# Optimization experiments

Measured on AMD Instinct MI355X. Metric: run time of the kernel, lower is better.

Reference implementation:

```python
import jax, jax.numpy as jnp
import numpy as np

NUM_EXPERTS = 8
RANK = 16
TOP_K = 2
SCALING = 32.0 / RANK  # alpha / rank = 2.0
IN_F = 2048
OUT_F = 2048


def setup_inputs() -> dict:
    key = jax.random.key(0)
    k1, k2, k3, k4, k5 = jax.random.split(key, 5)
    B, T = 4, 2048
    x = jax.random.normal(k1, (B, T, IN_F), dtype=jnp.float32)
    # kaiming-uniform-ish scales
    bound_w = 1.0 / np.sqrt(IN_F)
    weight = jax.random.uniform(k2, (OUT_F, IN_F), jnp.float32, -bound_w, bound_w)
    lora_A = jax.random.uniform(k3, (NUM_EXPERTS, RANK, IN_F), jnp.float32, -bound_w, bound_w)
    # lora_B is zero-initialized in the module; use small random values so the
    # expert path is numerically non-trivial for kernel correctness testing.
    lora_B = 0.02 * jax.random.normal(k4, (NUM_EXPERTS, OUT_F, RANK), dtype=jnp.float32)
    router_w = jax.random.uniform(k5, (NUM_EXPERTS, IN_F), jnp.float32, -bound_w, bound_w)
    return {"x": x, "weight": weight, "lora_A": lora_A, "lora_B": lora_B, "router_w": router_w}


def reference(x, weight, lora_A, lora_B, router_w):
    B, T, D = x.shape
    N = B * T
    # base dense projection: [B,T,O]
    base = jnp.einsum('btd,od->bto', x, weight)
    # routing
    logits = jnp.einsum('btd,ed->bte', x, router_w)
    probs = jax.nn.softmax(logits, axis=-1)
    topk_vals, topk_idx = jax.lax.top_k(probs, TOP_K)          # [B,T,K]
    topk_vals = topk_vals / topk_vals.sum(axis=-1, keepdims=True)
    # dense per-token expert weights: zero for non-selected experts -> same math
    # as the per-k gather loop (top_k indices are distinct).
    w_dense = jnp.zeros((N, NUM_EXPERTS), dtype=x.dtype).at[
        jnp.arange(N)[:, None], topk_idx.reshape(N, TOP_K)
    ].set(topk_vals.reshape(N, TOP_K))                          # [N,E]
    x_flat = x.reshape(N, D)
    # low-rank expert path: Ax [N,E,r] is tiny (E*r=128), then weighted combine
    Ax = jnp.einsum('nd,erd->ner', x_flat, lora_A)
    expert_out = jnp.einsum('ner,ne,eor->no', Ax, w_dense, lora_B) * SCALING
    return base + expert_out.reshape(B, T, OUT_F)
```

## Files before the change

### kernel.cpp

```cpp
#include <hip/hip_runtime.h>
#include <hip/hip_bf16.h>
#include <stdint.h>

#define IN_F   2048
#define OUT_F  2048
#define NTOK   8192
#define KAUG   2176
#define RANKE  128
#define SCALING 2.0f
#define NT64   34
#define NITER  17

typedef float  f32x4 __attribute__((ext_vector_type(4)));
typedef __bf16 bf16x8 __attribute__((ext_vector_type(8)));

#define GLOAD(g, l) __builtin_amdgcn_global_load_lds(                                   \
    (const __attribute__((address_space(1))) unsigned int*)(g),                          \
    (__attribute__((address_space(3))) unsigned int*)(l), 16, 0, 0)
#define PIN()    asm volatile("" ::: "memory")
#define BAR()    __builtin_amdgcn_s_barrier()
#define WAITL()  asm volatile("s_waitcnt lgkmcnt(0)" ::: "memory")
#define WAITV0() asm volatile("s_waitcnt vmcnt(0)" ::: "memory")
#define WAITV4() asm volatile("s_waitcnt vmcnt(4)" ::: "memory")
#define WAITV5() asm volatile("s_waitcnt vmcnt(5)" ::: "memory")
#define SB0()    __builtin_amdgcn_sched_barrier(0)

__device__ __forceinline__ unsigned short f2b(float f) {
  union { float f; unsigned u; } v; v.f = f;
  return (unsigned short)((v.u + 0x7FFFu + ((v.u >> 16) & 1u)) >> 16);
}

__device__ __forceinline__ uint4 pack8(float4 a, float4 b) {
  uint4 p;
  p.x = f2b(a.x) | ((unsigned)f2b(a.y) << 16);
  p.y = f2b(a.z) | ((unsigned)f2b(a.w) << 16);
  p.z = f2b(b.x) | ((unsigned)f2b(b.y) << 16);
  p.w = f2b(b.z) | ((unsigned)f2b(b.w) << 16);
  return p;
}

__device__ __forceinline__ uint2 pack4(float4 a) {
  uint2 p;
  p.x = f2b(a.x) | ((unsigned)f2b(a.y) << 16);
  p.y = f2b(a.z) | ((unsigned)f2b(a.w) << 16);
  return p;
}

__global__ __launch_bounds__(256)
void k_pre(const float* __restrict__ x, const float* __restrict__ rw,
           const float* __restrict__ wt, const float* __restrict__ lb,
           const float* __restrict__ la,
           unsigned short* __restrict__ Ap, float* __restrict__ wsc,
           unsigned short* __restrict__ Bp, unsigned short* __restrict__ Ac) {
  const int bid = blockIdx.x;
  const int t = threadIdx.x;

  if (bid >= 3072) {
    const int r0 = (bid - 3072) * 16;
    #pragma unroll
    for (int j = 0; j < 16; ++j) {
      int ch = j * 256 + t;
      int row = r0 + (ch >> 8), col8 = ch & 255;
      const float4* src = (const float4*)(la + (size_t)row * IN_F + col8 * 8);
      *(uint4*)(Ac + (size_t)row * IN_F + col8 * 8) = pack8(src[0], src[1]);
    }
    return;
  }
  if (bid >= 1024) {
    const int o = bid - 1024;
    const int c = t * 8;
    const float4* src = (const float4*)(wt + (size_t)o * IN_F + c);
    *(uint4*)(Bp + (size_t)o * KAUG + c) = pack8(src[0], src[1]);
    if (t < RANKE) {
      float v = lb[((size_t)(t >> 4) * OUT_F + o) * 16 + (t & 15)];
      Bp[(size_t)o * KAUG + IN_F + t] = f2b(v);
    }
    return;
  }

  const int w = t >> 6, l = t & 63;
  const int n0 = bid * 8 + w * 2;

  float4 xr[2][8];
  #pragma unroll
  for (int ti = 0; ti < 2; ++ti) {
    const float4* xp = (const float4*)(x + (size_t)(n0 + ti) * IN_F);
    uint2* dst = (uint2*)(Ap + (size_t)(n0 + ti) * KAUG);
    #pragma unroll
    for (int j = 0; j < 8; ++j) {
      float4 a = xp[j * 64 + l];
      xr[ti][j] = a;
      dst[j * 64 + l] = pack4(a);
    }
  }
  float acc[2][8];
  #pragma unroll
  for (int ti = 0; ti < 2; ++ti)
    #pragma unroll
    for (int e = 0; e < 8; ++e) acc[ti][e] = 0.f;
  #pragma unroll
  for (int e = 0; e < 8; ++e) {
    const float4* wp = (const float4*)(rw + (size_t)e * IN_F);
    #pragma unroll
    for (int j = 0; j < 8; ++j) {
      float4 b = wp[j * 64 + l];
      #pragma unroll
      for (int ti = 0; ti < 2; ++ti)
        acc[ti][e] += xr[ti][j].x * b.x + xr[ti][j].y * b.y +
                      xr[ti][j].z * b.z + xr[ti][j].w * b.w;
    }
  }
  #pragma unroll
  for (int ti = 0; ti < 2; ++ti)
    #pragma unroll
    for (int e = 0; e < 8; ++e) {
      #pragma unroll
      for (int msk = 1; msk <= 32; msk <<= 1) acc[ti][e] += __shfl_xor(acc[ti][e], msk);
    }
  #pragma unroll
  for (int ti = 0; ti < 2; ++ti) {
    float m = acc[ti][0];
    #pragma unroll
    for (int e = 1; e < 8; ++e) m = fmaxf(m, acc[ti][e]);
    float ex[8], dn = 0.f;
    #pragma unroll
    for (int e = 0; e < 8; ++e) { ex[e] = expf(acc[ti][e] - m); dn += ex[e]; }
    float inv = 1.f / dn;
    float v1 = -1.f; int i1 = 0;
    #pragma unroll
    for (int e = 0; e < 8; ++e) {
      float p = ex[e] * inv;
      if (p > v1) { v1 = p; i1 = e; }
    }
    float v2 = -1.f; int i2 = 0;
    #pragma unroll
    for (int e = 0; e < 8; ++e) {
      float p = ex[e] * inv;
      if (e != i1 && p > v2) { v2 = p; i2 = e; }
    }
    if ((l >> 3) == ti) {
      int e = l & 7;
      float wsum = v1 + v2;
      float wv = (e == i1) ? (v1 / wsum) : ((e == i2) ? (v2 / wsum) : 0.f);
      wsc[(size_t)(n0 + ti) * 8 + e] = wv * SCALING;
    }
  }
}

__global__ __launch_bounds__(256)
void k_lora(const unsigned short* __restrict__ Ap, const unsigned short* __restrict__ Ac,
            const float* __restrict__ wsc, unsigned short* __restrict__ Vout) {
  __shared__ alignas(16) unsigned short LA[3 * 2048];
  __shared__ alignas(16) unsigned short LB[3 * 8192];
  const int t = threadIdx.x, bm = blockIdx.x;
  const int w = t >> 6, l = t & 63;
  const int lr = l & 15, lq = l >> 4, lx = l & 7;
  const unsigned short* Ablk = Ap + (size_t)bm * 32 * KAUG;
  const int rr = t >> 3, cs = t & 7;
  const int sc = cs ^ (rr & 7);

  f32x4 acc[2][2];
  #pragma unroll
  for (int i = 0; i < 2; ++i)
    #pragma unroll
    for (int j = 0; j < 2; ++j) acc[i][j] = f32x4{0.f, 0.f, 0.f, 0.f};

  auto stg = [&](int buf, int kt) {
    GLOAD(Ablk + (size_t)rr * KAUG + kt * 64 + sc * 8, LA + buf * 2048 + w * 512);
    #pragma unroll
    for (int r = 0; r < 4; ++r)
      GLOAD(Ac + (size_t)(r * 32 + rr) * IN_F + kt * 64 + sc * 8,
            LB + buf * 8192 + r * 2048 + w * 512);
  };

  const int as0 = (lq ^ lx) * 8, as1 = ((4 + lq) ^ lx) * 8;

  stg(0, 0); stg(1, 1);
  for (int kt = 0; kt < 32; ++kt) {
    if (kt == 31) { WAITV0(); } else { WAITV5(); }
    PIN(); BAR();
    if (kt + 2 < 32) stg((kt + 2) % 3, kt + 2);
    const int buf = kt % 3;
    bf16x8 aF[2][2], bF[2][2];
    #pragma unroll
    for (int mi = 0; mi < 2; ++mi) {
      aF[mi][0] = *(const bf16x8*)(LA + buf * 2048 + lr * 64 + mi * 1024 + as0);
      aF[mi][1] = *(const bf16x8*)(LA + buf * 2048 + lr * 64 + mi * 1024 + as1);
    }
    #pragma unroll
    for (int ni = 0; ni < 2; ++ni) {
      bF[ni][0] = *(const bf16x8*)(LB + buf * 8192 + w * 2048 + lr * 64 + ni * 1024 + as0);
      bF[ni][1] = *(const bf16x8*)(LB + buf * 8192 + w * 2048 + lr * 64 + ni * 1024 + as1);
    }
    #pragma unroll
    for (int mi = 0; mi < 2; ++mi)
      #pragma unroll
      for (int ni = 0; ni < 2; ++ni)
        #pragma unroll
        for (int ks = 0; ks < 2; ++ks)
          acc[mi][ni] = __builtin_amdgcn_mfma_f32_16x16x32_bf16(aF[mi][ks], bF[ni][ks], acc[mi][ni], 0, 0, 0);
  }

  #pragma unroll
  for (int mi = 0; mi < 2; ++mi)
    #pragma unroll
    for (int ni = 0; ni < 2; ++ni)
      #pragma unroll
      for (int j = 0; j < 4; ++j) {
        int row = bm * 32 + mi * 16 + lq * 4 + j;
        int col = w * 32 + ni * 16 + lr;
        float sg = wsc[row * 8 + (col >> 4)];
        Vout[(size_t)row * KAUG + col] = f2b(acc[mi][ni][j] * sg);
      }
}

__global__ __launch_bounds__(512, 2)
void k_main(const unsigned short* __restrict__ A, const unsigned short* __restrict__ B,
            float* __restrict__ out) {
  __shared__ alignas(16) unsigned short LDS[65536];

  const int tid = threadIdx.x;
  const int id = blockIdx.x;
  const int wg = (id & 7) * 32 + (id >> 3);
  const int bn = wg >> 5, bm = wg & 31;
  const int w = tid >> 6, l = tid & 63;
  const int wr = w >> 2, wc = w & 3;
  const int lr = l & 15, lq = l >> 4, lx = l & 7;

  const unsigned short* Ablk = A + (size_t)bm * 256 * KAUG;
  const unsigned short* Bblk = B + (size_t)bn * 256 * KAUG;

  const size_t gofs0 = (size_t)(tid >> 3) * KAUG + (size_t)(((tid & 7) ^ ((tid >> 3) & 7)) * 8);
  const size_t gofs1 = (size_t)((tid + 512) >> 3) * KAUG +
                       (size_t)((((tid + 512) & 7) ^ (((tid + 512) >> 3) & 7)) * 8);
  unsigned short* const ldsW = LDS + w * 512;

  const int arow = wr * 128 + lr, brow = wc * 64 + lr;
  const int sl0 = (lq ^ lx) * 8, sl1 = ((4 + lq) ^ lx) * 8;

  f32x4 acc[8][4];
  #pragma unroll
  for (int i = 0; i < 8; ++i)
    #pragma unroll
    for (int j = 0; j < 4; ++j) acc[i][j] = f32x4{0.f, 0.f, 0.f, 0.f};
  bf16x8 aF[4][2], bF[4][2];

  auto stage = [&](int isB, int half, int kt) {
    if (kt >= NT64) return;
    const unsigned short* g = (isB ? Bblk : Ablk) + (size_t)(half * 128) * KAUG + (size_t)kt * 64;
    unsigned short* ld = ldsW + isB * 32768 + (kt & 1) * 16384 + half * 8192;
    GLOAD(g + gofs0, ld);
    GLOAD(g + gofs1, ld + 4096);
  };

#define QUAD(MQ, NQ)                                                                     \
  do {                                                                                   \
    _Pragma("unroll") for (int mi_ = 0; mi_ < 4; ++mi_)                                  \
    _Pragma("unroll") for (int ni_ = 0; ni_ < 2; ++ni_)                                  \
    _Pragma("unroll") for (int ks_ = 0; ks_ < 2; ++ks_)                                  \
      acc[(MQ)*4 + mi_][(NQ)*2 + ni_] = __builtin_amdgcn_mfma_f32_16x16x32_bf16(         \
          aF[mi_][ks_], bF[(NQ)*2 + ni_][ks_], acc[(MQ)*4 + mi_][(NQ)*2 + ni_],          \
          0, 0, 0);                                                                      \
  } while (0)

  stage(1, 0, 0); stage(1, 1, 0); stage(0, 0, 0); stage(0, 1, 0);
  stage(1, 0, 1); stage(1, 1, 1);
  WAITV4(); PIN(); BAR();

  for (int i = 0; i < NITER; ++i) {
    const int k1 = 2 * i + 1;
    const int a0 = arow * 64,   b0 = 32768 + brow * 64;
    const int a1 = a0 + 16384,  b1 = b0 + 16384;

    #pragma unroll
    for (int mi = 0; mi < 4; ++mi) {
      aF[mi][0] = *(const bf16x8*)(LDS + a0 + mi * 1024 + sl0);
      aF[mi][1] = *(const bf16x8*)(LDS + a0 + mi * 1024 + sl1);
    }
    #pragma unroll
    for (int ni = 0; ni < 2; ++ni) {
      bF[ni][0] = *(const bf16x8*)(LDS + b0 + ni * 1024 + sl0);
      bF[ni][1] = *(const bf16x8*)(LDS + b0 + ni * 1024 + sl1);
    }
    stage(0, 0, k1);
    PIN(); WAITL(); SB0();
    __builtin_amdgcn_s_setprio(1); QUAD(0, 0); __builtin_amdgcn_s_setprio(0);
    PIN(); BAR();
    #pragma unroll
    for (int ni = 2; ni < 4; ++ni) {
      bF[ni][0] = *(const bf16x8*)(LDS + b0 + ni * 1024 + sl0);
      bF[ni][1] = *(const bf16x8*)(LDS + b0 + ni * 1024 + sl1);
    }
    stage(0, 1, k1);
    PIN(); WAITL(); SB0();
    __builtin_amdgcn_s_setprio(1); QUAD(0, 1); __builtin_amdgcn_s_setprio(0);
    PIN(); BAR();
    #pragma unroll
    for (int mi = 0; mi < 4; ++mi) {
      aF[mi][0] = *(const bf16x8*)(LDS + a0 + (mi + 4) * 1024 + sl0);
      aF[mi][1] = *(const bf16x8*)(LDS + a0 + (mi + 4) * 1024 + sl1);
    }
    stage(1, 0, k1 + 1);
    PIN(); WAITL(); SB0();
    __builtin_amdgcn_s_setprio(1); QUAD(1, 1); __builtin_amdgcn_s_setprio(0);
    PIN(); BAR();
    stage(1, 1, k1 + 1);
    PIN();
    __builtin_amdgcn_s_setprio(1); QUAD(1, 0); __builtin_amdgcn_s_setprio(0);
    PIN();
    if (i == NITER - 1) { WAITV0(); } else { WAITV4(); }
    PIN(); BAR();

    #pragma unroll
    for (int mi = 0; mi < 4; ++mi) {
      aF[mi][0] = *(const bf16x8*)(LDS + a1 + mi * 1024 + sl0);
      aF[mi][1] = *(const bf16x8*)(LDS + a1 + mi * 1024 + sl1);
    }
    #pragma unroll
    for (int ni = 0; ni < 2; ++ni) {
      bF[ni][0] = *(const bf16x8*)(LDS + b1 + ni * 1024 + sl0);
      bF[ni][1] = *(const bf16x8*)(LDS + b1 + ni * 1024 + sl1);
    }
    stage(0, 0, k1 + 1);
    PIN(); WAITL(); SB0();
    __builtin_amdgcn_s_setprio(1); QUAD(0, 0); __builtin_amdgcn_s_setprio(0);
    PIN(); BAR();
    #pragma unroll
    for (int ni = 2; ni < 4; ++ni) {
      bF[ni][0] = *(const bf16x8*)(LDS + b1 + ni * 1024 + sl0);
      bF[ni][1] = *(const bf16x8*)(LDS + b1 + ni * 1024 + sl1);
    }
    stage(0, 1, k1 + 1);
    PIN(); WAITL(); SB0();
    __builtin_amdgcn_s_setprio(1); QUAD(0, 1); __builtin_amdgcn_s_setprio(0);
    PIN(); BAR();
    #pragma unroll
    for (int mi = 0; mi < 4; ++mi) {
      aF[mi][0] = *(const bf16x8*)(LDS + a1 + (mi + 4) * 1024 + sl0);
      aF[mi][1] = *(const bf16x8*)(LDS + a1 + (mi + 4) * 1024 + sl1);
    }
    stage(1, 0, k1 + 2);
    PIN(); WAITL(); SB0();
    __builtin_amdgcn_s_setprio(1); QUAD(1, 1); __builtin_amdgcn_s_setprio(0);
    PIN(); BAR();
    stage(1, 1, k1 + 2);
    PIN();
    __builtin_amdgcn_s_setprio(1); QUAD(1, 0); __builtin_amdgcn_s_setprio(0);
    PIN();
    if (i == NITER - 1) { WAITV0(); } else { WAITV4(); }
    PIN(); BAR();
  }
#undef QUAD

  #pragma unroll
  for (int mi = 0; mi < 8; ++mi)
    #pragma unroll
    for (int ni = 0; ni < 4; ++ni)
      #pragma unroll
      for (int j = 0; j < 4; ++j) {
        int row = bm * 256 + wr * 128 + mi * 16 + lq * 4 + j;
        int col = bn * 256 + wc * 64 + ni * 16 + lr;
        out[(size_t)row * OUT_F + col] = acc[mi][ni][j];
      }
}

extern "C" void kernel_launch(void* const* d_in, const int* in_sizes, int n_in,
                              void* d_out, int out_size, void* d_ws, size_t ws_size,
                              hipStream_t stream) {
  const float* x  = (const float*)d_in[0];
  const float* wt = (const float*)d_in[1];
  const float* la = (const float*)d_in[2];
  const float* lb = (const float*)d_in[3];
  const float* rw = (const float*)d_in[4];
  float* out = (float*)d_out;
  char* ws = (char*)d_ws;

  unsigned short* Ap  = (unsigned short*)ws;
  unsigned short* Bp  = (unsigned short*)(ws + 35651584);
  unsigned short* Ac  = (unsigned short*)(ws + 44564480);
  float*          wsc = (float*)(ws + 45088768);

  k_pre<<<3080, 256, 0, stream>>>(x, rw, wt, lb, la, Ap, wsc, Bp, Ac);
  k_lora<<<NTOK / 32, 256, 0, stream>>>(Ap, Ac, wsc, Ap + IN_F);
  k_main<<<256, 512, 0, stream>>>(Ap, Bp, out);
}
```

Baseline: 127.8 us.

## Fuse routing, weight conversion and LoRA-A projection into one prep kernel

Merges the preprocessing kernel and the LoRA down-projection kernel into a single 256-block kernel. Each block converts 32 token rows of x to bf16, stages them in LDS and computes router softmax/top-2 in shared memory. It then projects those rows through lora_A, which is streamed from fp32 and converted on the fly. This removes one launch, the bf16 copy of lora_A, the gate-weight buffer, and the re-read of x from global memory. The cost is heavy LDS use (~145KB per block), only 256 blocks doing serialized work, and every block re-reading all of lora_A from global memory with register prefetch instead of async loads.

```diff
diff --git a/kernel.cpp b/kernel.cpp
--- a/kernel.cpp
+++ b/kernel.cpp
@@ -22,7 +22,6 @@
 #define WAITL()  asm volatile("s_waitcnt lgkmcnt(0)" ::: "memory")
 #define WAITV0() asm volatile("s_waitcnt vmcnt(0)" ::: "memory")
 #define WAITV4() asm volatile("s_waitcnt vmcnt(4)" ::: "memory")
-#define WAITV5() asm volatile("s_waitcnt vmcnt(5)" ::: "memory")
 #define SB0()    __builtin_amdgcn_sched_barrier(0)
 
 __device__ __forceinline__ unsigned short f2b(float f) {
@@ -47,170 +46,165 @@
 }
 
 __global__ __launch_bounds__(256)
-void k_pre(const float* __restrict__ x, const float* __restrict__ rw,
-           const float* __restrict__ wt, const float* __restrict__ lb,
-           const float* __restrict__ la,
-           unsigned short* __restrict__ Ap, float* __restrict__ wsc,
-           unsigned short* __restrict__ Bp, unsigned short* __restrict__ Ac) {
-  const int bid = blockIdx.x;
+void k_prep(const float* __restrict__ x, const float* __restrict__ rw,
+            const float* __restrict__ wt, const float* __restrict__ lb,
+            const float* __restrict__ la,
+            unsigned short* __restrict__ Ap, unsigned short* __restrict__ Bp) {
+  __shared__ alignas(16) unsigned short xs[32 * 2048];
+  __shared__ alignas(16) unsigned short as_[128 * 64];
+  __shared__ float ws[32][8];
+
+  const int pb = blockIdx.x;
   const int t = threadIdx.x;
-
-  if (bid >= 3072) {
-    const int r0 = (bid - 3072) * 16;
-    #pragma unroll
-    for (int j = 0; j < 16; ++j) {
-      int ch = j * 256 + t;
-      int row = r0 + (ch >> 8), col8 = ch & 255;
-      const float4* src = (const float4*)(la + (size_t)row * IN_F + col8 * 8);
-      *(uint4*)(Ac + (size_t)row * IN_F + col8 * 8) = pack8(src[0], src[1]);
-    }
-    return;
-  }
-  if (bid >= 1024) {
-    const int o = bid - 1024;
-    const int c = t * 8;
-    const float4* src = (const float4*)(wt + (size_t)o * IN_F + c);
-    *(uint4*)(Bp + (size_t)o * KAUG + c) = pack8(src[0], src[1]);
+  const int w = t >> 6, l = t & 63;
+  const int n0 = pb * 32;
+
+  for (int p = 0; p < 4; ++p) {
+    const int tk0 = w * 8 + p * 2;
+    float4 xr[2][8];
+    #pragma unroll
+    for (int ti = 0; ti < 2; ++ti) {
+      const int row = tk0 + ti;
+      const float4* xp = (const float4*)(x + (size_t)(n0 + row) * IN_F);
+      uint2* dst = (uint2*)(Ap + (size_t)(n0 + row) * KAUG);
+      #pragma unroll
+      for (int j = 0; j < 8; ++j) {
+        int idx = j * 64 + l;
+        float4 a = xp[idx];
+        xr[ti][j] = a;
+        uint2 pk = pack4(a);
+        dst[idx] = pk;
+        *(uint2*)((char*)xs + row * 4096 + (((idx >> 1) ^ (row & 7)) << 4) + (idx & 1) * 8) = pk;
+      }
+    }
+    float acc[2][8];
+    #pragma unroll
+    for (int ti = 0; ti < 2; ++ti)
+      #pragma unroll
+      for (int e = 0; e < 8; ++e) acc[ti][e] = 0.f;
+    #pragma unroll
+    for (int e = 0; e < 8; ++e) {
+      const float4* wp = (const float4*)(rw + (size_t)e * IN_F);
+      #pragma unroll
+      for (int j = 0; j < 8; ++j) {
+        float4 b = wp[j * 64 + l];
+        #pragma unroll
+        for (int ti = 0; ti < 2; ++ti)
+          acc[ti][e] += xr[ti][j].x * b.x + xr[ti][j].y * b.y +
+                        xr[ti][j].z * b.z + xr[ti][j].w * b.w;
+      }
+    }
+    #pragma unroll
+    for (int ti = 0; ti < 2; ++ti)
+      #pragma unroll
+      for (int e = 0; e < 8; ++e) {
+        #pragma unroll
+        for (int msk = 1; msk <= 32; msk <<= 1) acc[ti][e] += __shfl_xor(acc[ti][e], msk);
+      }
+    #pragma unroll
+    for (int ti = 0; ti < 2; ++ti) {
+      float m = acc[ti][0];
+      #pragma unroll
+      for (int e = 1; e < 8; ++e) m = fmaxf(m, acc[ti][e]);
+      float ex[8], dn = 0.f;
+      #pragma unroll
+      for (int e = 0; e < 8; ++e) { ex[e] = expf(acc[ti][e] - m); dn += ex[e]; }
+      float inv = 1.f / dn;
+      float v1 = -1.f; int i1 = 0;
+      #pragma unroll
+      for (int e = 0; e < 8; ++e) {
+        float pr = ex[e] * inv;
+        if (pr > v1) { v1 = pr; i1 = e; }
+      }
+      float v2 = -1.f; int i2 = 0;
+      #pragma unroll
+      for (int e = 0; e < 8; ++e) {
+        float pr = ex[e] * inv;
+        if (e != i1 && pr > v2) { v2 = pr; i2 = e; }
+      }
+      if ((l >> 3) == ti) {
+        int e = l & 7;
+        float wsum = v1 + v2;
+        float wv = (e == i1) ? (v1 / wsum) : ((e == i2) ? (v2 / wsum) : 0.f);
+        ws[tk0 + ti][e] = wv * SCALING;
+      }
+    }
+  }
+
+  #pragma unroll
+  for (int i = 0; i < 8; ++i) {
+    const int o = pb * 8 + i;
+    const float4* src = (const float4*)(wt + (size_t)o * IN_F + t * 8);
+    *(uint4*)(Bp + (size_t)o * KAUG + t * 8) = pack8(src[0], src[1]);
     if (t < RANKE) {
       float v = lb[((size_t)(t >> 4) * OUT_F + o) * 16 + (t & 15)];
       Bp[(size_t)o * KAUG + IN_F + t] = f2b(v);
     }
-    return;
-  }
-
-  const int w = t >> 6, l = t & 63;
-  const int n0 = bid * 8 + w * 2;
-
-  float4 xr[2][8];
-  #pragma unroll
-  for (int ti = 0; ti < 2; ++ti) {
-    const float4* xp = (const float4*)(x + (size_t)(n0 + ti) * IN_F);
-    uint2* dst = (uint2*)(Ap + (size_t)(n0 + ti) * KAUG);
-    #pragma unroll
-    for (int j = 0; j < 8; ++j) {
-      float4 a = xp[j * 64 + l];
-      xr[ti][j] = a;
-      dst[j * 64 + l] = pack4(a);
-    }
-  }
-  float acc[2][8];
-  #pragma unroll
-  for (int ti = 0; ti < 2; ++ti)
-    #pragma unroll
-    for (int e = 0; e < 8; ++e) acc[ti][e] = 0.f;
-  #pragma unroll
-  for (int e = 0; e < 8; ++e) {
-    const float4* wp = (const float4*)(rw + (size_t)e * IN_F);
-    #pragma unroll
-    for (int j = 0; j < 8; ++j) {
-      float4 b = wp[j * 64 + l];
-      #pragma unroll
-      for (int ti = 0; ti < 2; ++ti)
-        acc[ti][e] += xr[ti][j].x * b.x + xr[ti][j].y * b.y +
-                      xr[ti][j].z * b.z + xr[ti][j].w * b.w;
-    }
-  }
-  #pragma unroll
-  for (int ti = 0; ti < 2; ++ti)
-    #pragma unroll
-    for (int e = 0; e < 8; ++e) {
-      #pragma unroll
-      for (int msk = 1; msk <= 32; msk <<= 1) acc[ti][e] += __shfl_xor(acc[ti][e], msk);
-    }
-  #pragma unroll
-  for (int ti = 0; ti < 2; ++ti) {
-    float m = acc[ti][0];
-    #pragma unroll
-    for (int e = 1; e < 8; ++e) m = fmaxf(m, acc[ti][e]);
-    float ex[8], dn = 0.f;
-    #pragma unroll
-    for (int e = 0; e < 8; ++e) { ex[e] = expf(acc[ti][e] - m); dn += ex[e]; }
-    float inv = 1.f / dn;
-    float v1 = -1.f; int i1 = 0;
-    #pragma unroll
-    for (int e = 0; e < 8; ++e) {
-      float p = ex[e] * inv;
-      if (p > v1) { v1 = p; i1 = e; }
-    }
-    float v2 = -1.f; int i2 = 0;
-    #pragma unroll
-    for (int e = 0; e < 8; ++e) {
-      float p = ex[e] * inv;
-      if (e != i1 && p > v2) { v2 = p; i2 = e; }
-    }
-    if ((l >> 3) == ti) {
-      int e = l & 7;
-      float wsum = v1 + v2;
-      float wv = (e == i1) ? (v1 / wsum) : ((e == i2) ? (v2 / wsum) : 0.f);
-      wsc[(size_t)(n0 + ti) * 8 + e] = wv * SCALING;
-    }
-  }
-}
-
-__global__ __launch_bounds__(256)
-void k_lora(const unsigned short* __restrict__ Ap, const unsigned short* __restrict__ Ac,
-            const float* __restrict__ wsc, unsigned short* __restrict__ Vout) {
-  __shared__ alignas(16) unsigned short LA[3 * 2048];
-  __shared__ alignas(16) unsigned short LB[3 * 8192];
-  const int t = threadIdx.x, bm = blockIdx.x;
-  const int w = t >> 6, l = t & 63;
-  const int lr = l & 15, lq = l >> 4, lx = l & 7;
-  const unsigned short* Ablk = Ap + (size_t)bm * 32 * KAUG;
-  const int rr = t >> 3, cs = t & 7;
-  const int sc = cs ^ (rr & 7);
-
-  f32x4 acc[2][2];
+  }
+
+  f32x4 vacc[2][2];
   #pragma unroll
   for (int i = 0; i < 2; ++i)
     #pragma unroll
-    for (int j = 0; j < 2; ++j) acc[i][j] = f32x4{0.f, 0.f, 0.f, 0.f};
-
-  auto stg = [&](int buf, int kt) {
-    GLOAD(Ablk + (size_t)rr * KAUG + kt * 64 + sc * 8, LA + buf * 2048 + w * 512);
-    #pragma unroll
-    for (int r = 0; r < 4; ++r)
-      GLOAD(Ac + (size_t)(r * 32 + rr) * IN_F + kt * 64 + sc * 8,
-            LB + buf * 8192 + r * 2048 + w * 512);
-  };
-
-  const int as0 = (lq ^ lx) * 8, as1 = ((4 + lq) ^ lx) * 8;
-
-  stg(0, 0); stg(1, 1);
+    for (int j = 0; j < 2; ++j) vacc[i][j] = f32x4{0.f, 0.f, 0.f, 0.f};
+  const int lr = l & 15, lq = l >> 4;
+
+  float4 abuf[8];
+  #pragma unroll
+  for (int i = 0; i < 8; ++i) {
+    int fi = i * 256 + t, r = fi >> 4, kq = fi & 15;
+    abuf[i] = ((const float4*)la)[r * 512 + kq];
+  }
   for (int kt = 0; kt < 32; ++kt) {
-    if (kt == 31) { WAITV0(); } else { WAITV5(); }
-    PIN(); BAR();
-    if (kt + 2 < 32) stg((kt + 2) % 3, kt + 2);
-    const int buf = kt % 3;
-    bf16x8 aF[2][2], bF[2][2];
-    #pragma unroll
-    for (int mi = 0; mi < 2; ++mi) {
-      aF[mi][0] = *(const bf16x8*)(LA + buf * 2048 + lr * 64 + mi * 1024 + as0);
-      aF[mi][1] = *(const bf16x8*)(LA + buf * 2048 + lr * 64 + mi * 1024 + as1);
-    }
-    #pragma unroll
-    for (int ni = 0; ni < 2; ++ni) {
-      bF[ni][0] = *(const bf16x8*)(LB + buf * 8192 + w * 2048 + lr * 64 + ni * 1024 + as0);
-      bF[ni][1] = *(const bf16x8*)(LB + buf * 8192 + w * 2048 + lr * 64 + ni * 1024 + as1);
-    }
+    #pragma unroll
+    for (int i = 0; i < 8; ++i) {
+      int fi = i * 256 + t, r = fi >> 4, kq = fi & 15;
+      *(uint2*)((char*)as_ + r * 128 + (((kq >> 1) ^ (r & 7)) << 4) + (kq & 1) * 8) = pack4(abuf[i]);
+    }
+    if (kt + 1 < 32) {
+      #pragma unroll
+      for (int i = 0; i < 8; ++i) {
+        int fi = i * 256 + t, r = fi >> 4, kq = fi & 15;
+        abuf[i] = ((const float4*)la)[r * 512 + (kt + 1) * 16 + kq];
+      }
+    }
+    __syncthreads();
+    bf16x8 xf[2][2], bf[2][2];
+    #pragma unroll
+    for (int mi = 0; mi < 2; ++mi)
+      #pragma unroll
+      for (int ks = 0; ks < 2; ++ks) {
+        int row = lr + mi * 16;
+        int ch = kt * 8 + ks * 4 + lq;
+        xf[mi][ks] = *(const bf16x8*)((char*)xs + row * 4096 + ((ch ^ (row & 7)) << 4));
+      }
+    #pragma unroll
+    for (int ni = 0; ni < 2; ++ni)
+      #pragma unroll
+      for (int ks = 0; ks < 2; ++ks) {
+        int r = w * 32 + ni * 16 + lr;
+        int ch = ks * 4 + lq;
+        bf[ni][ks] = *(const bf16x8*)((char*)as_ + r * 128 + ((ch ^ (r & 7)) << 4));
+      }
     #pragma unroll
     for (int mi = 0; mi < 2; ++mi)
       #pragma unroll
       for (int ni = 0; ni < 2; ++ni)
         #pragma unroll
         for (int ks = 0; ks < 2; ++ks)
-          acc[mi][ni] = __builtin_amdgcn_mfma_f32_16x16x32_bf16(aF[mi][ks], bF[ni][ks], acc[mi][ni], 0, 0, 0);
-  }
-
+          vacc[mi][ni] = __builtin_amdgcn_mfma_f32_16x16x32_bf16(xf[mi][ks], bf[ni][ks], vacc[mi][ni], 0, 0, 0);
+    __syncthreads();
+  }
   #pragma unroll
   for (int mi = 0; mi < 2; ++mi)
     #pragma unroll
     for (int ni = 0; ni < 2; ++ni)
       #pragma unroll
       for (int j = 0; j < 4; ++j) {
-        int row = bm * 32 + mi * 16 + lq * 4 + j;
+        int row = mi * 16 + lq * 4 + j;
         int col = w * 32 + ni * 16 + lr;
-        float sg = wsc[row * 8 + (col >> 4)];
-        Vout[(size_t)row * KAUG + col] = f2b(acc[mi][ni][j] * sg);
+        float g = ws[row][w * 2 + ni];
+        Ap[(size_t)(n0 + row) * KAUG + IN_F + col] = f2b(vacc[mi][ni][j] * g);
       }
 }
 
@@ -377,10 +371,7 @@
 
   unsigned short* Ap  = (unsigned short*)ws;
   unsigned short* Bp  = (unsigned short*)(ws + 35651584);
-  unsigned short* Ac  = (unsigned short*)(ws + 44564480);
-  float*          wsc = (float*)(ws + 45088768);
-
-  k_pre<<<3080, 256, 0, stream>>>(x, rw, wt, lb, la, Ap, wsc, Bp, Ac);
-  k_lora<<<NTOK / 32, 256, 0, stream>>>(Ap, Ac, wsc, Ap + IN_F);
+
+  k_prep<<<256, 256, 0, stream>>>(x, rw, wt, lb, la, Ap, Bp);
   k_main<<<256, 512, 0, stream>>>(Ap, Bp, out);
 }
```

Measured after the change: 128.0 us. No clear change (+0.2%).
